# Kernel tuning notes

Measured on AMD Instinct MI355X. Metric: run time of the kernel, lower is better.

Reference implementation:

```python
import jax, jax.numpy as jnp
import numpy as np

HIDDEN = 1024
N_HEADS = 16
HEAD_DIM = HIDDEN // N_HEADS  # 64
B, N = 2, 2048
SCALE = HIDDEN ** (-0.5)  # NOTE: original scales by full hidden_size, not head_dim


def setup_inputs() -> dict:
    key = jax.random.key(0)
    k1, k2 = jax.random.split(key)
    hidden_states = jax.random.normal(k1, (B, N, HIDDEN), dtype=jnp.float32)
    attention_mask = jnp.ones((B, N), dtype=jnp.int32)
    # per-head no-bias Linear(hidden -> 3*head_dim), stacked: [h, hidden, 3*head_dim]
    W_qkv = jax.random.normal(k2, (N_HEADS, HIDDEN, 3 * HEAD_DIM), dtype=jnp.float32) * (HIDDEN ** -0.5)
    return {"hidden_states": hidden_states, "attention_mask": attention_mask, "W_qkv": W_qkv}


def reference(hidden_states, attention_mask, W_qkv):
    # qkv: [b, h, n, 3*d]
    qkv = jnp.einsum('bnD,hDe->bhne', hidden_states, W_qkv)
    q, k, v = jnp.split(qkv, 3, axis=-1)  # each [b, h, n, d]
    scores = jnp.einsum('bhid,bhjd->bhij', q, k) * SCALE
    mask = attention_mask[:, None, None, :] == 0  # [b,1,1,n]
    scores = jnp.where(mask, -jnp.inf, scores)
    attn = jax.nn.softmax(scores, axis=-1)
    out = jnp.einsum('bhij,bhjd->bhid', attn, v)  # [b, h, n, d]
    # rearrange 'b h n d -> b n (h d)'
    return jnp.transpose(out, (0, 2, 1, 3)).reshape(out.shape[0], out.shape[2], -1)
```

## Files before the change

kernel.cpp:

```cpp
#include <hip/hip_runtime.h>
#include <hip/hip_bf16.h>


#define NH   16
#define HD   64
#define SEQ  2048
#define HID  1024
#define E3   192
#define QSCALE 0.04508422017f
#define MBIAS  -43.2808512f

typedef __attribute__((ext_vector_type(8))) short short8;
typedef __attribute__((ext_vector_type(4))) float f32x4;
typedef __attribute__((ext_vector_type(16))) float f32x16;
typedef unsigned short ushort_t;

#define MFMA16(a, b, c) __builtin_amdgcn_mfma_f32_16x16x32_bf16((a), (b), (c), 0, 0, 0)
#define MFMA32(a, b, c) __builtin_amdgcn_mfma_f32_32x32x16_bf16((a), (b), (c), 0, 0, 0)

#if __has_builtin(__builtin_amdgcn_exp2f)
#define EXP2(x) __builtin_amdgcn_exp2f(x)
#else
#define EXP2(x) exp2f(x)
#endif

static __device__ __forceinline__ ushort_t f2bf(float x) {
    unsigned u = __builtin_bit_cast(unsigned, x);
    unsigned r = u + 0x7fff + ((u >> 16) & 1);
    return (ushort_t)(r >> 16);
}

static __device__ __forceinline__ unsigned pack_trunc(float hi, float lo) {
#if __has_builtin(__builtin_amdgcn_perm)
    return __builtin_amdgcn_perm(__builtin_bit_cast(unsigned, hi),
                                 __builtin_bit_cast(unsigned, lo), 0x07060302u);
#else
    return (__builtin_bit_cast(unsigned, hi) & 0xffff0000u) |
           (__builtin_bit_cast(unsigned, lo) >> 16);
#endif
}

static __device__ __forceinline__ void load_lds16(const void* g, void* l) {
    __builtin_amdgcn_global_load_lds(
        (__attribute__((address_space(1))) void*)(g),
        (__attribute__((address_space(3))) void*)(l), 16, 0, 0);
}

__global__ __launch_bounds__(256) void k_cvt_x(const void* __restrict__ Xv,
                                               ushort_t* __restrict__ Xb,
                                               int* __restrict__ flagp) {
    __shared__ int cnt;
    if (threadIdx.x == 0) cnt = 0;
    __syncthreads();
    const unsigned* X32 = (const unsigned*)Xv;
    if (threadIdx.x < 64) {
        unsigned u = X32[(size_t)blockIdx.x * 2048 + threadIdx.x * 32 + 7];
        int bexp = (u >> 7) & 0xFF;
        if (bexp >= 0x68 && bexp <= 0x90) atomicAdd(&cnt, 1);
    }
    __syncthreads();
    const int isf32 = (cnt < 32);
    if (blockIdx.x == 0 && threadIdx.x == 0) *flagp = isf32;

    const size_t base = ((size_t)blockIdx.x * 256 + threadIdx.x) * 16;
    if (isf32) {
        const float* Xf = (const float*)Xv;
        ushort_t tmp[16];
#pragma unroll
        for (int c = 0; c < 4; ++c) {
            float4 v = *(const float4*)(Xf + base + c * 4);
            tmp[c * 4 + 0] = f2bf(v.x); tmp[c * 4 + 1] = f2bf(v.y);
            tmp[c * 4 + 2] = f2bf(v.z); tmp[c * 4 + 3] = f2bf(v.w);
        }
        *(float4*)(Xb + base)     = ((const float4*)tmp)[0];
        *(float4*)(Xb + base + 8) = ((const float4*)tmp)[1];
    } else {
        const ushort_t* Xh = (const ushort_t*)Xv;
        *(float4*)(Xb + base)     = *(const float4*)(Xh + base);
        *(float4*)(Xb + base + 8) = *(const float4*)(Xh + base + 8);
    }
}

__global__ __launch_bounds__(256) void k_cvt_w(const void* __restrict__ Wv,
                                               ushort_t* __restrict__ Wt,
                                               const int* __restrict__ flagp) {
    __shared__ ushort_t tile[64][72];
    const int isf32 = *flagp;
    const int h  = blockIdx.x;
    const int dt = blockIdx.y;
    const int et = blockIdx.z;
    const int D0 = dt * 64, e0 = et * 64;
    const int t  = threadIdx.x;
#pragma unroll
    for (int r = 0; r < 2; ++r) {
        int row = r * 32 + (t >> 3);
        int col = (t & 7) * 8;
        size_t base = ((size_t)(h * HID + D0 + row)) * E3 + e0 + col;
        if (isf32) {
            const float* Wf = (const float*)Wv;
            float4 a = *(const float4*)(Wf + base);
            float4 c = *(const float4*)(Wf + base + 4);
            tile[row][col + 0] = f2bf(a.x); tile[row][col + 1] = f2bf(a.y);
            tile[row][col + 2] = f2bf(a.z); tile[row][col + 3] = f2bf(a.w);
            tile[row][col + 4] = f2bf(c.x); tile[row][col + 5] = f2bf(c.y);
            tile[row][col + 6] = f2bf(c.z); tile[row][col + 7] = f2bf(c.w);
        } else {
            *(float4*)&tile[row][col] = *(const float4*)((const ushort_t*)Wv + base);
        }
    }
    __syncthreads();
#pragma unroll
    for (int r = 0; r < 2; ++r) {
        int erow = r * 32 + (t >> 3);
        int dcol = (t & 7) * 8;
        ushort_t vals[8];
#pragma unroll
        for (int i = 0; i < 8; ++i) vals[i] = tile[dcol + i][erow];
        *(float4*)(Wt + ((size_t)(h * E3 + e0 + erow)) * HID + D0 + dcol) = *(float4*)vals;
    }
}

__global__ __launch_bounds__(256) void k_qkv(const ushort_t* __restrict__ Xb,
                                             const ushort_t* __restrict__ Wt,
                                             ushort_t* __restrict__ Qb,
                                             ushort_t* __restrict__ Kb,
                                             ushort_t* __restrict__ Vtb) {
    __shared__ __align__(16) ushort_t smem[2 * 128 * 64];
    ushort_t* Xl = smem;
    ushort_t* Wl = smem + 128 * 64;

    const int e0 = blockIdx.x * 128;
    const int m0 = blockIdx.y * 128;
    const int b  = m0 >> 11;
    const int n0 = m0 & 2047;
    const int t = threadIdx.x;
    const int w = t >> 6, lane = t & 63, l15 = lane & 15, quad = lane >> 4;
    const int wrow0 = (w & 1) * 64, wcol0 = (w >> 1) * 64;
    const int srow = lane >> 3;
    const int scb  = (lane & 7) ^ srow;

    f32x4 acc[4][4];
#pragma unroll
    for (int i = 0; i < 4; ++i)
#pragma unroll
        for (int j = 0; j < 4; ++j) acc[i][j] = (f32x4){0.f, 0.f, 0.f, 0.f};

    for (int k0 = 0; k0 < HID; k0 += 64) {
        __syncthreads();
#pragma unroll
        for (int cc = 0; cc < 4; ++cc) {
            const int ch  = w * 4 + cc;
            const int row = ch * 8 + srow;
            load_lds16(Xb + (size_t)(m0 + row) * HID + k0 + scb * 8, &Xl[ch * 512]);
            load_lds16(Wt + (size_t)(e0 + row) * HID + k0 + scb * 8, &Wl[ch * 512]);
        }
        __syncthreads();
#pragma unroll
        for (int kh = 0; kh < 2; ++kh) {
            short8 af[4], bfm[4];
#pragma unroll
            for (int i = 0; i < 4; ++i) {
                const int r = wrow0 + i * 16 + l15;
                af[i] = *(const short8*)&Xl[r * 64 + ((kh * 4 + quad) ^ (r & 7)) * 8];
            }
#pragma unroll
            for (int j = 0; j < 4; ++j) {
                const int r = wcol0 + j * 16 + l15;
                bfm[j] = *(const short8*)&Wl[r * 64 + ((kh * 4 + quad) ^ (r & 7)) * 8];
            }
#pragma unroll
            for (int i = 0; i < 4; ++i)
#pragma unroll
                for (int j = 0; j < 4; ++j)
                    acc[i][j] = MFMA16(af[i], bfm[j], acc[i][j]);
        }
    }

    ushort_t* Vbuf = smem;
    __syncthreads();
#pragma unroll
    for (int i = 0; i < 4; ++i) {
#pragma unroll
        for (int j = 0; j < 4; ++j) {
            const int E0v = e0 + wcol0 + j * 16;
            const int hh  = E0v / 192;
            const int r0  = E0v - hh * 192;
            const int bh  = b * NH + hh;
            const int nb  = n0 + wrow0 + i * 16 + quad * 4;
            if (r0 < 64) {
                const int e = r0 + l15;
#pragma unroll
                for (int reg = 0; reg < 4; ++reg)
                    Qb[((size_t)bh * SEQ + nb + reg) * HD + e] = f2bf(acc[i][j][reg] * QSCALE);
            } else if (r0 < 128) {
                const int e = r0 - 64 + l15;
#pragma unroll
                for (int reg = 0; reg < 4; ++reg)
                    Kb[((size_t)bh * SEQ + nb + reg) * HD + e] = f2bf(acc[i][j][reg]);
            } else {
                const int d  = r0 - 128 + l15;
                const int nl = wrow0 + i * 16 + quad * 4;
#pragma unroll
                for (int reg = 0; reg < 4; ++reg)
                    Vbuf[d * 136 + nl + reg] = f2bf(acc[i][j][reg]);
            }
        }
    }
    const int m3 = blockIdx.x % 3;
    if (m3 != 0) {
        __syncthreads();
        const int hv  = (e0 + ((m3 == 1) ? 0 : 64)) / 192;
        const int bhv = b * NH + hv;
        const int dr = t >> 2, part = t & 3;
        size_t dst = ((size_t)bhv * HD + dr) * SEQ + n0 + part * 32;
#pragma unroll
        for (int c = 0; c < 4; ++c) {
            float4 v = *(const float4*)&Vbuf[dr * 136 + part * 32 + c * 8];
            *(float4*)(Vtb + dst + c * 8) = v;
        }
    }
}


#define SMPACK(sv, h0v, h1v)                                                  \
    {                                                                         \
        _Pragma("unroll")                                                     \
        for (int g = 0; g < 4; ++g) {                                         \
            float p0 = EXP2(sv[4*g+0]); float p1 = EXP2(sv[4*g+1]);           \
            float p2 = EXP2(sv[4*g+2]); float p3 = EXP2(sv[4*g+3]);           \
            l_r += (p0 + p1) + (p2 + p3);                                     \
            unsigned a0 = pack_trunc(p1, p0), a1 = pack_trunc(p3, p2);        \
            unsigned b0 = a0, b1 = a1;                                        \
            asm volatile("v_permlane32_swap_b32 %0, %1" : "+v"(a0), "+v"(b0));\
            asm volatile("v_permlane32_swap_b32 %0, %1" : "+v"(a1), "+v"(b1));\
            h0v[g*2+0] = a0; h1v[g*2+0] = b0;                                 \
            h0v[g*2+1] = a1; h1v[g*2+1] = b1;                                 \
        }                                                                     \
    }

#define MAKE_PB(dst, h0v, h1v, GB)                                            \
    {                                                                         \
        unsigned w0_ = hi ? h0v[(GB+1)*2+0] : h0v[(GB)*2+0];                  \
        unsigned w1_ = hi ? h0v[(GB+1)*2+1] : h0v[(GB)*2+1];                  \
        unsigned w2_ = hi ? h1v[(GB+1)*2+0] : h1v[(GB)*2+0];                  \
        unsigned w3_ = hi ? h1v[(GB+1)*2+1] : h1v[(GB)*2+1];                  \
        uint4 u_ = {w0_, w1_, w2_, w3_};                                      \
        dst = __builtin_bit_cast(short8, u_);                                 \
    }

__global__ __launch_bounds__(512, 4) void k_attn(const ushort_t* __restrict__ Qb,
                                                 const ushort_t* __restrict__ Kb,
                                                 const ushort_t* __restrict__ Vtb,
                                                 const int* __restrict__ mask,
                                                 void* __restrict__ outv,
                                                 const int* __restrict__ flagp) {
    __shared__ __align__(16) char smem_raw[57344];
    float* biasl = (float*)(smem_raw + 49152);

    const int isf32 = *flagp;
    const int q0 = blockIdx.x * 128;
    const int bh = blockIdx.y;
    const int b  = bh >> 4, h = bh & 15;
    const int t  = threadIdx.x;
    const int w  = t >> 6, lane = t & 63;
    const int wq = w >> 1, jh = w & 1;
    const int c31 = lane & 31, hi = lane >> 5;
    const int srow = lane >> 3;
    const int scb  = (lane & 7) ^ srow;
    const int rx7  = c31 & 7;

#pragma unroll
    for (int tj = 0; tj < 2; ++tj) {
        ushort_t* kb = (ushort_t*)(smem_raw + tj * 16384);
        ushort_t* vb = kb + 4096;
        load_lds16(Kb  + ((size_t)bh * SEQ + tj * 64 + w * 8 + srow) * HD + scb * 8, &kb[w * 512]);
        load_lds16(Vtb + ((size_t)bh * HD + w * 8 + srow) * SEQ + tj * 64 + scb * 8, &vb[w * 512]);
    }

    int lm = 0;
    for (int i = t; i < SEQ; i += 512) {
        int mv = mask[b * SEQ + i];
        biasl[i] = mv ? 0.0f : MBIAS;
        lm |= (mv == 0);
    }
    const int qrow = q0 + wq * 32 + c31;
    short8 qB[4];
#pragma unroll
    for (int ds = 0; ds < 4; ++ds)
        qB[ds] = *(const short8*)(Qb + ((size_t)bh * SEQ + qrow) * HD + ds * 16 + hi * 8);

    const int use_bias = __syncthreads_or(lm);

    const f32x16 z16 = {0.f,0.f,0.f,0.f,0.f,0.f,0.f,0.f,0.f,0.f,0.f,0.f,0.f,0.f,0.f,0.f};
    f32x16 oa = z16, ob = z16;
    float l_r = 0.f;

    const int jrow = jh * 32 + c31;

    for (int j0 = 0; j0 < SEQ; j0 += 64) {
        const int idx = (j0 >> 6) % 3;
        if (j0 + 64 < SEQ) { asm volatile("s_waitcnt vmcnt(2)" ::: "memory"); }
        else               { asm volatile("s_waitcnt vmcnt(0)" ::: "memory"); }
        __builtin_amdgcn_s_barrier();
        asm volatile("" ::: "memory");
        if (j0 + 128 < SEQ) {
            ushort_t* kb2 = (ushort_t*)(smem_raw + ((idx + 2) % 3) * 16384);
            ushort_t* vb2 = kb2 + 4096;
            load_lds16(Kb  + ((size_t)bh * SEQ + j0 + 128 + w * 8 + srow) * HD + scb * 8, &kb2[w * 512]);
            load_lds16(Vtb + ((size_t)bh * HD + w * 8 + srow) * SEQ + j0 + 128 + scb * 8, &vb2[w * 512]);
        }
        ushort_t* kb = (ushort_t*)(smem_raw + idx * 16384);
        ushort_t* vb = kb + 4096;

        short8 kf0 = *(const short8*)&kb[jrow * 64 + ((0 + hi) ^ rx7) * 8];
        f32x16 s = MFMA32(kf0, qB[0], z16);
#pragma unroll
        for (int ds = 1; ds < 4; ++ds) {
            short8 kf = *(const short8*)&kb[jrow * 64 + ((2 * ds + hi) ^ rx7) * 8];
            s = MFMA32(kf, qB[ds], s);
        }
        if (use_bias) {
#pragma unroll
            for (int g = 0; g < 4; ++g) {
                float4 bj = *(const float4*)&biasl[j0 + jh * 32 + 8 * g + 4 * hi];
                s[4*g+0] += bj.x; s[4*g+1] += bj.y; s[4*g+2] += bj.z; s[4*g+3] += bj.w;
            }
        }

        unsigned h0[8], h1[8];
        SMPACK(s, h0, h1);

#pragma unroll
        for (int c13 = 0; c13 < 2; ++c13) {
            short8 pb;
            MAKE_PB(pb, h0, h1, 2 * c13);
            const int cbase = 2 * (jh * 2 + c13) + hi;
            short8 va0 = *(const short8*)&vb[(c31)      * 64 + (cbase ^ rx7) * 8];
            short8 va1 = *(const short8*)&vb[(32 + c31) * 64 + (cbase ^ rx7) * 8];
            oa = MFMA32(va0, pb, oa);
            ob = MFMA32(va1, pb, ob);
        }
    }

    float l_h = l_r + __shfl_xor(l_r, 32);

    __syncthreads();
    float* Obuf = (float*)smem_raw;
    float* Lbuf = (float*)(smem_raw + 49152);
    const int slot = (wq * 64 + lane) * 36;
    if (jh == 1) {
#pragma unroll
        for (int g = 0; g < 4; ++g) {
            *(float4*)&Obuf[slot + g * 4]      = (float4){oa[4*g], oa[4*g+1], oa[4*g+2], oa[4*g+3]};
            *(float4*)&Obuf[slot + 16 + g * 4] = (float4){ob[4*g], ob[4*g+1], ob[4*g+2], ob[4*g+3]};
        }
        Lbuf[wq * 64 + lane] = l_h;
    }
    __syncthreads();
    float rinv = 0.f;
    if (jh == 0) {
        const float l_tot = l_h + Lbuf[wq * 64 + lane];
        rinv = 1.0f / l_tot;
#pragma unroll
        for (int g = 0; g < 4; ++g) {
            float4 pa = *(const float4*)&Obuf[slot + g * 4];
            float4 pb4 = *(const float4*)&Obuf[slot + 16 + g * 4];
            oa[4*g] += pa.x; oa[4*g+1] += pa.y; oa[4*g+2] += pa.z; oa[4*g+3] += pa.w;
            ob[4*g] += pb4.x; ob[4*g+1] += pb4.y; ob[4*g+2] += pb4.z; ob[4*g+3] += pb4.w;
        }
    }
    __syncthreads();

    const int qlr = wq * 32 + c31;
    const int r = t >> 2, part = t & 3;
    if (!isf32) {
        ushort_t* Ol = (ushort_t*)smem_raw;
        if (jh == 0) {
#pragma unroll
            for (int dt = 0; dt < 2; ++dt) {
                const f32x16 ov = dt ? ob : oa;
#pragma unroll
                for (int g = 0; g < 4; ++g) {
                    const int d0 = dt * 32 + 8 * g + 4 * hi;
                    uint2 u;
                    u.x = (unsigned)f2bf(ov[4*g+0] * rinv) | ((unsigned)f2bf(ov[4*g+1] * rinv) << 16);
                    u.y = (unsigned)f2bf(ov[4*g+2] * rinv) | ((unsigned)f2bf(ov[4*g+3] * rinv) << 16);
                    *(uint2*)&Ol[qlr * 72 + d0] = u;
                }
            }
        }
        __syncthreads();
        ushort_t* outp = (ushort_t*)outv;
        size_t dst = ((size_t)b * SEQ + q0 + r) * HID + h * HD + part * 16;
        float4 v0 = *(const float4*)&Ol[r * 72 + part * 16];
        float4 v1 = *(const float4*)&Ol[r * 72 + part * 16 + 8];
        *(float4*)(outp + dst)     = v0;
        *(float4*)(outp + dst + 8) = v1;
    } else {
        float* Olf = (float*)smem_raw;
        if (jh == 0) {
#pragma unroll
            for (int dt = 0; dt < 2; ++dt) {
                const f32x16 ov = dt ? ob : oa;
#pragma unroll
                for (int g = 0; g < 4; ++g) {
                    const int d0 = dt * 32 + 8 * g + 4 * hi;
                    float4 fv;
                    fv.x = ov[4*g+0] * rinv; fv.y = ov[4*g+1] * rinv;
                    fv.z = ov[4*g+2] * rinv; fv.w = ov[4*g+3] * rinv;
                    *(float4*)&Olf[qlr * 68 + d0] = fv;
                }
            }
        }
        __syncthreads();
        float* outp = (float*)outv;
        size_t dst = ((size_t)b * SEQ + q0 + r) * HID + h * HD + part * 16;
#pragma unroll
        for (int c = 0; c < 4; ++c) {
            float4 v = *(const float4*)&Olf[r * 68 + part * 16 + c * 4];
            *(float4*)(outp + dst + c * 4) = v;
        }
    }
}

extern "C" void kernel_launch(void* const* d_in, const int* in_sizes, int n_in,
                              void* d_out, int out_size, void* d_ws, size_t ws_size,
                              hipStream_t stream) {
    const void* X    = d_in[0];
    const int*  mask = (const int*)d_in[1];
    const void* W    = d_in[2];

    char* ws = (char*)d_ws;
    ushort_t* Qb    = (ushort_t*)(ws);
    ushort_t* Kb    = (ushort_t*)(ws + 8388608);
    ushort_t* Vtb   = (ushort_t*)(ws + 16777216);
    ushort_t* Wtb   = (ushort_t*)(ws + 25165824);
    int*      flagp = (int*)(ws + 31457280);
    ushort_t* Xb    = (ushort_t*)d_out;

    k_cvt_x<<<1024, 256, 0, stream>>>(X, Xb, flagp);
    k_cvt_w<<<dim3(16, 16, 3), 256, 0, stream>>>(W, Wtb, flagp);
    k_qkv<<<dim3(24, 32), 256, 0, stream>>>(Xb, Wtb, Qb, Kb, Vtb);
    k_attn<<<dim3(16, 32), 512, 0, stream>>>(Qb, Kb, Vtb, mask, d_out, flagp);
}
```

Before: 175.3 us.

## Process 128-key tiles with double buffering and MFMA priority hints in attention

The key/value tile grows from 64 to 128 keys per iteration, and the triple-buffered LDS ring becomes a double buffer of 32KB tiles. The V-transpose tile switches to a 16-way XOR swizzle to match its wider rows. Each wave now computes two 32x32 score blocks per iteration, and the MFMA sections are wrapped in s_setprio hints. This halves the number of barriers and loop iterations, but LDS use grows to 72KB, which may limit occupancy at launch_bounds(512,4). The wait now drains all outstanding loads (vmcnt(0)) each iteration, so prefetch overlap shrinks to a single tile ahead.

New measurement: 176.3 us. Within noise of the previous version (+0.6%).

```diff
diff --git a/kernel.cpp b/kernel.cpp
--- a/kernel.cpp
+++ b/kernel.cpp
@@ -254,8 +254,8 @@
                                                  const int* __restrict__ mask,
                                                  void* __restrict__ outv,
                                                  const int* __restrict__ flagp) {
-    __shared__ __align__(16) char smem_raw[57344];
-    float* biasl = (float*)(smem_raw + 49152);
+    __shared__ __align__(16) char smem_raw[73728];
+    float* biasl = (float*)(smem_raw + 65536);
 
     const int isf32 = *flagp;
     const int q0 = blockIdx.x * 128;
@@ -265,16 +265,25 @@
     const int w  = t >> 6, lane = t & 63;
     const int wq = w >> 1, jh = w & 1;
     const int c31 = lane & 31, hi = lane >> 5;
-    const int srow = lane >> 3;
-    const int scb  = (lane & 7) ^ srow;
-    const int rx7  = c31 & 7;
-
-#pragma unroll
-    for (int tj = 0; tj < 2; ++tj) {
-        ushort_t* kb = (ushort_t*)(smem_raw + tj * 16384);
-        ushort_t* vb = kb + 4096;
-        load_lds16(Kb  + ((size_t)bh * SEQ + tj * 64 + w * 8 + srow) * HD + scb * 8, &kb[w * 512]);
-        load_lds16(Vtb + ((size_t)bh * HD + w * 8 + srow) * SEQ + tj * 64 + scb * 8, &vb[w * 512]);
+    const int srow8 = lane >> 3;
+    const int scb   = (lane & 7) ^ srow8;
+    const int vrow4 = lane >> 4;
+    const int vb15  = lane & 15;
+    const int rx7   = c31 & 7;
+    const int rx15  = c31 & 15;
+
+    {
+        ushort_t* kb = (ushort_t*)(smem_raw);
+        ushort_t* vb = (ushort_t*)(smem_raw + 16384);
+#pragma unroll
+        for (int c = 0; c < 2; ++c) {
+            const int krow = w * 16 + c * 8 + srow8;
+            load_lds16(Kb + ((size_t)bh * SEQ + krow) * HD + scb * 8,
+                       &kb[(w * 2 + c) * 512]);
+            const int vrow = w * 8 + c * 4 + vrow4;
+            load_lds16(Vtb + ((size_t)bh * HD + vrow) * SEQ + ((vb15 ^ (vrow & 15)) * 8),
+                       &vb[(w * 2 + c) * 512]);
+        }
     }
 
     int lm = 0;
@@ -295,58 +304,76 @@
     f32x16 oa = z16, ob = z16;
     float l_r = 0.f;
 
-    const int jrow = jh * 32 + c31;
-
-    for (int j0 = 0; j0 < SEQ; j0 += 64) {
-        const int idx = (j0 >> 6) % 3;
-        if (j0 + 64 < SEQ) { asm volatile("s_waitcnt vmcnt(2)" ::: "memory"); }
-        else               { asm volatile("s_waitcnt vmcnt(0)" ::: "memory"); }
+    for (int j0 = 0; j0 < SEQ; j0 += 128) {
+        const int idx = (j0 >> 7) & 1;
+        asm volatile("s_waitcnt vmcnt(0)" ::: "memory");
         __builtin_amdgcn_s_barrier();
         asm volatile("" ::: "memory");
         if (j0 + 128 < SEQ) {
-            ushort_t* kb2 = (ushort_t*)(smem_raw + ((idx + 2) % 3) * 16384);
-            ushort_t* vb2 = kb2 + 4096;
-            load_lds16(Kb  + ((size_t)bh * SEQ + j0 + 128 + w * 8 + srow) * HD + scb * 8, &kb2[w * 512]);
-            load_lds16(Vtb + ((size_t)bh * HD + w * 8 + srow) * SEQ + j0 + 128 + scb * 8, &vb2[w * 512]);
-        }
-        ushort_t* kb = (ushort_t*)(smem_raw + idx * 16384);
-        ushort_t* vb = kb + 4096;
-
-        short8 kf0 = *(const short8*)&kb[jrow * 64 + ((0 + hi) ^ rx7) * 8];
-        f32x16 s = MFMA32(kf0, qB[0], z16);
-#pragma unroll
-        for (int ds = 1; ds < 4; ++ds) {
-            short8 kf = *(const short8*)&kb[jrow * 64 + ((2 * ds + hi) ^ rx7) * 8];
-            s = MFMA32(kf, qB[ds], s);
-        }
+            ushort_t* kb2 = (ushort_t*)(smem_raw + (idx ^ 1) * 32768);
+            ushort_t* vb2 = kb2 + 8192;
+#pragma unroll
+            for (int c = 0; c < 2; ++c) {
+                const int krow = w * 16 + c * 8 + srow8;
+                load_lds16(Kb + ((size_t)bh * SEQ + j0 + 128 + krow) * HD + scb * 8,
+                           &kb2[(w * 2 + c) * 512]);
+                const int vrow = w * 8 + c * 4 + vrow4;
+                load_lds16(Vtb + ((size_t)bh * HD + vrow) * SEQ + j0 + 128 + ((vb15 ^ (vrow & 15)) * 8),
+                           &vb2[(w * 2 + c) * 512]);
+            }
+        }
+        ushort_t* kb = (ushort_t*)(smem_raw + idx * 32768);
+        ushort_t* vb = kb + 8192;
+
+        const int jr0 = jh * 64 + c31;
+        const int jr1 = jh * 64 + 32 + c31;
+        f32x16 s0, s1;
+        __builtin_amdgcn_s_setprio(1);
+#pragma unroll
+        for (int ds = 0; ds < 4; ++ds) {
+            short8 kf0 = *(const short8*)&kb[jr0 * 64 + (((2 * ds + hi) ^ rx7) * 8)];
+            short8 kf1 = *(const short8*)&kb[jr1 * 64 + (((2 * ds + hi) ^ rx7) * 8)];
+            s0 = MFMA32(kf0, qB[ds], ds ? s0 : z16);
+            s1 = MFMA32(kf1, qB[ds], ds ? s1 : z16);
+        }
+        __builtin_amdgcn_s_setprio(0);
         if (use_bias) {
 #pragma unroll
             for (int g = 0; g < 4; ++g) {
-                float4 bj = *(const float4*)&biasl[j0 + jh * 32 + 8 * g + 4 * hi];
-                s[4*g+0] += bj.x; s[4*g+1] += bj.y; s[4*g+2] += bj.z; s[4*g+3] += bj.w;
-            }
-        }
-
-        unsigned h0[8], h1[8];
-        SMPACK(s, h0, h1);
-
-#pragma unroll
-        for (int c13 = 0; c13 < 2; ++c13) {
-            short8 pb;
-            MAKE_PB(pb, h0, h1, 2 * c13);
-            const int cbase = 2 * (jh * 2 + c13) + hi;
-            short8 va0 = *(const short8*)&vb[(c31)      * 64 + (cbase ^ rx7) * 8];
-            short8 va1 = *(const short8*)&vb[(32 + c31) * 64 + (cbase ^ rx7) * 8];
-            oa = MFMA32(va0, pb, oa);
-            ob = MFMA32(va1, pb, ob);
-        }
+                float4 bj0 = *(const float4*)&biasl[j0 + jh * 64 + 8 * g + 4 * hi];
+                float4 bj1 = *(const float4*)&biasl[j0 + jh * 64 + 32 + 8 * g + 4 * hi];
+                s0[4*g+0] += bj0.x; s0[4*g+1] += bj0.y; s0[4*g+2] += bj0.z; s0[4*g+3] += bj0.w;
+                s1[4*g+0] += bj1.x; s1[4*g+1] += bj1.y; s1[4*g+2] += bj1.z; s1[4*g+3] += bj1.w;
+            }
+        }
+
+        unsigned h0a[8], h1a[8], h0b[8], h1b[8];
+        SMPACK(s0, h0a, h1a);
+        SMPACK(s1, h0b, h1b);
+
+        __builtin_amdgcn_s_setprio(1);
+#pragma unroll
+        for (int half = 0; half < 2; ++half) {
+#pragma unroll
+            for (int c13 = 0; c13 < 2; ++c13) {
+                short8 pb;
+                if (half == 0) { MAKE_PB(pb, h0a, h1a, 2 * c13); }
+                else           { MAKE_PB(pb, h0b, h1b, 2 * c13); }
+                const int pblk = (jh * 4 + half * 2 + c13) * 2 + hi;
+                short8 va0 = *(const short8*)&vb[(c31)      * 128 + ((pblk ^ rx15) * 8)];
+                short8 va1 = *(const short8*)&vb[(32 + c31) * 128 + ((pblk ^ rx15) * 8)];
+                oa = MFMA32(va0, pb, oa);
+                ob = MFMA32(va1, pb, ob);
+            }
+        }
+        __builtin_amdgcn_s_setprio(0);
     }
 
     float l_h = l_r + __shfl_xor(l_r, 32);
 
     __syncthreads();
     float* Obuf = (float*)smem_raw;
-    float* Lbuf = (float*)(smem_raw + 49152);
+    float* Lbuf = (float*)(smem_raw + 65536);
     const int slot = (wq * 64 + lane) * 36;
     if (jh == 1) {
 #pragma unroll
```
